# Performance work log

Hardware: AMD Instinct MI355X
Metric: run time of the kernel (lower is better)

The kernel has to match this reference:

```python
import jax, jax.numpy as jnp
import numpy as np
import math

D_MODEL = 1024
NUM_HEADS = 16
N_GROUP = 4
HEAD_DIM = D_MODEL // NUM_HEADS  # 64
KV_DIM = N_GROUP * HEAD_DIM      # 256
BS, SEQ = 2, 2048


def setup_inputs() -> dict:
    key = jax.random.key(0)
    ks = jax.random.split(key, 7)
    s = 0.02
    return {
        "h": jax.random.normal(ks[0], (BS, SEQ, D_MODEL), dtype=jnp.float32),
        "wq_w": jax.random.normal(ks[1], (D_MODEL, D_MODEL), dtype=jnp.float32) * s,
        "wq_b": jnp.zeros((D_MODEL,), dtype=jnp.float32),
        "wk_w": jax.random.normal(ks[2], (KV_DIM, D_MODEL), dtype=jnp.float32) * s,
        "wk_b": jnp.zeros((KV_DIM,), dtype=jnp.float32),
        "wv_w": jax.random.normal(ks[3], (KV_DIM, D_MODEL), dtype=jnp.float32) * s,
        "wv_b": jnp.zeros((KV_DIM,), dtype=jnp.float32),
    }


def reference(h, wq_w, wq_b, wk_w, wk_b, wv_w, wv_b):
    bs, seq, _ = h.shape
    rep = NUM_HEADS // N_GROUP  # heads per KV group

    # Linear projections (torch Linear: x @ W.T + b)
    q = h @ wq_w.T + wq_b                     # [bs, seq, d_model]
    k = h @ wk_w.T + wk_b                     # [bs, seq, kv_dim]
    v = h @ wv_w.T + wv_b                     # [bs, seq, kv_dim]

    q = q.reshape(bs, seq, NUM_HEADS, HEAD_DIM).transpose(0, 2, 1, 3)  # [b,H,s,d]
    k = k.reshape(bs, seq, N_GROUP, HEAD_DIM)                          # [b,s,G,d]
    v = v.reshape(bs, seq, N_GROUP, HEAD_DIM)
    # torch .repeat(1,1,1,rep).view(...,num_heads,head_dim) maps head h -> group h//rep,
    # identical to repeating each group `rep` times consecutively along the head axis.
    k = jnp.repeat(k, rep, axis=2).transpose(0, 2, 1, 3)               # [b,H,s,d]
    v = jnp.repeat(v, rep, axis=2).transpose(0, 2, 1, 3)               # [b,H,s,d]

    scores = jnp.einsum("bhqd,bhkd->bhqk", q, k) / math.sqrt(HEAD_DIM)
    attn = jax.nn.softmax(scores, axis=-1)
    out = jnp.einsum("bhqk,bhkd->bhqd", attn, v)                       # [b,H,s,d]
    out = out.transpose(0, 2, 1, 3).reshape(bs, seq, NUM_HEADS * HEAD_DIM)
    return out
```

## Files before the change

### kernel.cpp

```cpp
#include <hip/hip_runtime.h>

typedef _Float16 f16;
typedef _Float16 f16x8 __attribute__((ext_vector_type(8)));
typedef _Float16 f16x4 __attribute__((ext_vector_type(4)));
typedef float f32x4 __attribute__((ext_vector_type(4)));

#define MFMA16(a, b, c) __builtin_amdgcn_mfma_f32_16x16x32_f16((a), (b), (c), 0, 0, 0)

#define SEQ 2048
#define DMODEL 1024
#define NH 16
#define NG 4
#define PAD 76

__device__ __forceinline__ f16x8 cvt8(const float4 a, const float4 b) {
    f16x8 r;
    r[0] = (f16)a.x; r[1] = (f16)a.y; r[2] = (f16)a.z; r[3] = (f16)a.w;
    r[4] = (f16)b.x; r[5] = (f16)b.y; r[6] = (f16)b.z; r[7] = (f16)b.w;
    return r;
}

__device__ __forceinline__ void gl_lds16(f16* lds, const f16* g) {
    __builtin_amdgcn_global_load_lds(
        (const __attribute__((address_space(1))) void*)g,
        (__attribute__((address_space(3))) void*)lds, 16, 0, 0);
}

#define HN  (4096 * 1024)
#define WQN (1024 * 1024)
#define WKN (256 * 1024)
#define WVN (256 * 1024)
#define TOT8 ((HN + WQN + WKN + WVN) / 8)

__global__ __launch_bounds__(256) void cvt_kernel(const float* __restrict__ h,
                                                  const float* __restrict__ wq,
                                                  const float* __restrict__ wk,
                                                  const float* __restrict__ wv,
                                                  f16* __restrict__ h16,
                                                  f16* __restrict__ W16) {
    const int c = blockIdx.x * 256 + threadIdx.x;
    if (c >= TOT8) return;
    const size_t e = (size_t)c * 8;
    const float* src;
    f16* dst;
    if (e < HN) {
        src = h + e; dst = h16 + e;
    } else {
        const size_t e2 = e - HN;
        if (e2 < WQN)            src = wq + e2;
        else if (e2 < WQN + WKN) src = wk + (e2 - WQN);
        else                     src = wv + (e2 - WQN - WKN);
        dst = W16 + e2;
    }
    const float4 a = *(const float4*)src;
    const float4 b = *(const float4*)(src + 4);
    *(f16x8*)dst = cvt8(a, b);
}

__global__ __launch_bounds__(256, 3) void qkv_gemm16(const f16* __restrict__ A,
                                                     const f16* __restrict__ W,
                                                     const float* __restrict__ bq,
                                                     const float* __restrict__ bk,
                                                     const float* __restrict__ bv,
                                                     f16* __restrict__ Qb,
                                                     f16* __restrict__ Kb,
                                                     f16* __restrict__ Vtb,
                                                     float qscale) {
    __shared__ __align__(16) f16 As[2][64 * 32];
    __shared__ __align__(16) f16 Bs[2][128 * 32];

    const int tid  = threadIdx.x;
    const int lane = tid & 63;
    const int l15  = lane & 15;
    const int l4   = lane >> 4;
    const int wave = tid >> 6;
    const int wm   = (wave >> 1) * 32;
    const int wn   = (wave & 1) * 64;
    const int bx   = blockIdx.x;
    const int m0   = blockIdx.y * 64;
    const int n0g  = bx * 128;

    const f16* Ag = A + ((size_t)(m0 + (lane >> 2))) * 1024 + (lane & 3) * 8;
    const f16* Wg = W + ((size_t)(n0g + (lane >> 2))) * 1024 + (lane & 3) * 8;
    const size_t rstep = (size_t)16 * 1024;

    f32x4 acc[2][4];
#pragma unroll
    for (int i = 0; i < 2; i++)
#pragma unroll
        for (int j = 0; j < 4; j++) acc[i][j] = (f32x4)0.0f;

    gl_lds16(&As[0][wave * 512],        Ag + (size_t)wave * rstep);
    gl_lds16(&Bs[0][wave * 1024],       Wg + (size_t)(wave * 2) * rstep);
    gl_lds16(&Bs[0][wave * 1024 + 512], Wg + (size_t)(wave * 2 + 1) * rstep);

    int cur = 0;
    for (int k0 = 0; k0 < DMODEL; k0 += 32) {
        __syncthreads();
        if (k0 + 32 < DMODEL) {
            const int nxt = cur ^ 1;
            const int kn = k0 + 32;
            gl_lds16(&As[nxt][wave * 512],        Ag + (size_t)wave * rstep + kn);
            gl_lds16(&Bs[nxt][wave * 1024],       Wg + (size_t)(wave * 2) * rstep + kn);
            gl_lds16(&Bs[nxt][wave * 1024 + 512], Wg + (size_t)(wave * 2 + 1) * rstep + kn);
        }

        const f16* Ab = As[cur];
        const f16* Bb = Bs[cur];
        f16x8 af[2], bf[4];
#pragma unroll
        for (int i = 0; i < 2; i++)
            af[i] = *(const f16x8*)&Ab[(wm + i * 16 + l15) * 32 + l4 * 8];
#pragma unroll
        for (int j = 0; j < 4; j++)
            bf[j] = *(const f16x8*)&Bb[(wn + j * 16 + l15) * 32 + l4 * 8];
        __builtin_amdgcn_s_setprio(1);
#pragma unroll
        for (int i = 0; i < 2; i++)
#pragma unroll
            for (int j = 0; j < 4; j++)
                acc[i][j] = MFMA16(af[i], bf[j], acc[i][j]);
        __builtin_amdgcn_s_setprio(0);
        cur ^= 1;
    }

    const float* bias; f16* C; int N, n0; float osc; int vmode;
    if (bx < 8)       { bias = bq; C = Qb;  N = 1024; n0 = bx * 128;        osc = qscale; vmode = 0; }
    else if (bx < 10) { bias = bk; C = Kb;  N = 256;  n0 = (bx - 8) * 128;  osc = 1.0f;   vmode = 0; }
    else              { bias = bv; C = Vtb; N = 256;  n0 = (bx - 10) * 128; osc = 1.0f;   vmode = 1; }

#pragma unroll
    for (int i = 0; i < 2; i++) {
        const int mbase = m0 + wm + i * 16 + l4 * 4;
#pragma unroll
        for (int j = 0; j < 4; j++) {
            const int n  = n0 + wn + j * 16 + l15;
            const float bb = bias[n];
            if (vmode == 0) {
#pragma unroll
                for (int r = 0; r < 4; r++)
                    C[(size_t)(mbase + r) * N + n] = (f16)((acc[i][j][r] + bb) * osc);
            } else {
                f16x4 p;
#pragma unroll
                for (int r = 0; r < 4; r++)
                    p[r] = (f16)((acc[i][j][r] + bb) * osc);
                const int batch = mbase >> 11;
                const int s     = mbase & 2047;
                *(f16x4*)&C[((size_t)(batch * 256 + n)) * SEQ + s] = p;
            }
        }
    }
}

__global__ __launch_bounds__(256, 2) void attn_kernel(const f16* __restrict__ Q,
                                                      const f16* __restrict__ Kt,
                                                      const f16* __restrict__ Vt,
                                                      float* __restrict__ out) {
    __shared__ __align__(16) f16 Ks[64 * PAD];
    __shared__ __align__(16) f16 Vs[64 * PAD];
    __shared__ __align__(16) f16 Ps[128 * PAD];

    const int tid  = threadIdx.x;
    const int lane = tid & 63;
    const int l15  = lane & 15;
    const int l4   = lane >> 4;
    const int wave = tid >> 6;
    const int b    = blockIdx.z;
    const int hh   = blockIdx.y;
    const int g    = hh >> 2;
    const int q0   = blockIdx.x * 128;
    const int qw   = wave * 32;

    f16x8 qf[2][2];
#pragma unroll
    for (int rg = 0; rg < 2; rg++)
#pragma unroll
        for (int kt = 0; kt < 2; kt++)
            qf[rg][kt] = *(const f16x8*)&Q[((size_t)(b * SEQ + q0 + qw + rg * 16 + l15)) * DMODEL
                                           + hh * 64 + kt * 32 + l4 * 8];

    f32x4 oacc[2][4];
    float lsum[2] = {0.0f, 0.0f};
#pragma unroll
    for (int rg = 0; rg < 2; rg++)
#pragma unroll
        for (int dt = 0; dt < 4; dt++) oacc[rg][dt] = (f32x4)0.0f;

    const int srow = tid >> 2;
    const int sc8  = (tid & 3) * 8;
    const f16* Kg = Kt + (size_t)(b * SEQ + srow) * 256 + g * 64 + sc8;
    const f16* Vg = Vt + (size_t)(b * 256 + g * 64 + srow) * SEQ + sc8;

    for (int kb = 0; kb < SEQ; kb += 64) {
        *(f16x8*)&Ks[srow * PAD + sc8]      = *(const f16x8*)(Kg + (size_t)kb * 256);
        *(f16x8*)&Ks[srow * PAD + 32 + sc8] = *(const f16x8*)(Kg + (size_t)kb * 256 + 32);
        *(f16x8*)&Vs[srow * PAD + sc8]      = *(const f16x8*)(Vg + kb);
        *(f16x8*)&Vs[srow * PAD + 32 + sc8] = *(const f16x8*)(Vg + kb + 32);
        __syncthreads();

        f32x4 sacc[2][4];
#pragma unroll
        for (int rg = 0; rg < 2; rg++)
#pragma unroll
            for (int jt = 0; jt < 4; jt++) sacc[rg][jt] = (f32x4)0.0f;
#pragma unroll
        for (int jt = 0; jt < 4; jt++) {
            const f16x8 kf0 = *(const f16x8*)&Ks[(jt * 16 + l15) * PAD + l4 * 8];
            const f16x8 kf1 = *(const f16x8*)&Ks[(jt * 16 + l15) * PAD + 32 + l4 * 8];
#pragma unroll
            for (int rg = 0; rg < 2; rg++) {
                sacc[rg][jt] = MFMA16(kf0, qf[rg][0], sacc[rg][jt]);
                sacc[rg][jt] = MFMA16(kf1, qf[rg][1], sacc[rg][jt]);
            }
        }

#pragma unroll
        for (int rg = 0; rg < 2; rg++)
#pragma unroll
            for (int jt = 0; jt < 4; jt++) {
                f16x4 pp;
#pragma unroll
                for (int r = 0; r < 4; r++) {
                    const float p = exp2f(fminf(sacc[rg][jt][r], 14.0f));
                    lsum[rg] += p;
                    pp[r] = (f16)p;
                }
                *(f16x4*)&Ps[(qw + rg * 16 + l15) * PAD + jt * 16 + l4 * 4] = pp;
            }

#pragma unroll
        for (int kt = 0; kt < 2; kt++) {
            const f16x8 pf0 = *(const f16x8*)&Ps[(qw + l15) * PAD + kt * 32 + l4 * 8];
            const f16x8 pf1 = *(const f16x8*)&Ps[(qw + 16 + l15) * PAD + kt * 32 + l4 * 8];
#pragma unroll
            for (int dt = 0; dt < 4; dt++) {
                const f16x8 vf = *(const f16x8*)&Vs[(dt * 16 + l15) * PAD + kt * 32 + l4 * 8];
                oacc[0][dt] = MFMA16(pf0, vf, oacc[0][dt]);
                oacc[1][dt] = MFMA16(pf1, vf, oacc[1][dt]);
            }
        }
        __syncthreads();
    }

#pragma unroll
    for (int rg = 0; rg < 2; rg++) {
        lsum[rg] += __shfl_xor(lsum[rg], 16);
        lsum[rg] += __shfl_xor(lsum[rg], 32);
    }

#pragma unroll
    for (int rg = 0; rg < 2; rg++)
#pragma unroll
        for (int r = 0; r < 4; r++) {
            const float lv  = __shfl(lsum[rg], l4 * 4 + r);
            const float inv = 1.0f / lv;
            const int q = q0 + qw + rg * 16 + l4 * 4 + r;
            float* op = out + ((size_t)(b * SEQ + q)) * DMODEL + hh * 64;
#pragma unroll
            for (int dt = 0; dt < 4; dt++)
                op[dt * 16 + l15] = oacc[rg][dt][r] * inv;
        }
}

extern "C" void kernel_launch(void* const* d_in, const int* in_sizes, int n_in,
                              void* d_out, int out_size, void* d_ws, size_t ws_size,
                              hipStream_t stream) {
    const float* h    = (const float*)d_in[0];
    const float* wq_w = (const float*)d_in[1];
    const float* wq_b = (const float*)d_in[2];
    const float* wk_w = (const float*)d_in[3];
    const float* wk_b = (const float*)d_in[4];
    const float* wv_w = (const float*)d_in[5];
    const float* wv_b = (const float*)d_in[6];
    float* out = (float*)d_out;

    char* ws = (char*)d_ws;
    f16* Qb  = (f16*)(ws + 0);
    f16* Kb  = (f16*)(ws + 8388608);
    f16* Vtb = (f16*)(ws + 10485760);
    f16* h16 = (f16*)(ws + 12582912);
    f16* W16 = (f16*)(ws + 20971520);

    const float qscale = 0.125f * 1.4426950408889634f;

    cvt_kernel<<<dim3(TOT8 / 256), 256, 0, stream>>>(h, wq_w, wk_w, wv_w, h16, W16);
    qkv_gemm16<<<dim3(12, 64), 256, 0, stream>>>(h16, W16, wq_b, wk_b, wv_b,
                                                 Qb, Kb, Vtb, qscale);
    attn_kernel<<<dim3(16, 16, 2), 256, 0, stream>>>(Qb, Kb, Vtb, out);
}
```

Baseline: 182.0 us.

## Double-buffer K/V tiles in attention kernel with register prefetch

Splits the K and V shared-memory tiles into two buffers. The next tile is loaded from global memory into registers at the start of each iteration, while the current tile is used for the QK and PV MFMAs, and is written to the other buffer afterward. One __syncthreads per iteration is removed and load latency is meant to be hidden behind compute. The cost is more LDS (about 19KB extra per block) and 16 extra VGPRs, which could affect occupancy at 2 blocks per CU.

```diff
diff --git a/kernel.cpp b/kernel.cpp
--- a/kernel.cpp
+++ b/kernel.cpp
@@ -157,8 +157,8 @@
                                                       const f16* __restrict__ Kt,
                                                       const f16* __restrict__ Vt,
                                                       float* __restrict__ out) {
-    __shared__ __align__(16) f16 Ks[64 * PAD];
-    __shared__ __align__(16) f16 Vs[64 * PAD];
+    __shared__ __align__(16) f16 Ks[2][64 * PAD];
+    __shared__ __align__(16) f16 Vs[2][64 * PAD];
     __shared__ __align__(16) f16 Ps[128 * PAD];
 
     const int tid  = threadIdx.x;
@@ -192,12 +192,28 @@
     const f16* Kg = Kt + (size_t)(b * SEQ + srow) * 256 + g * 64 + sc8;
     const f16* Vg = Vt + (size_t)(b * 256 + g * 64 + srow) * SEQ + sc8;
 
+    {
+        const f16x8 k0 = *(const f16x8*)(Kg);
+        const f16x8 k1 = *(const f16x8*)(Kg + 32);
+        const f16x8 v0 = *(const f16x8*)(Vg);
+        const f16x8 v1 = *(const f16x8*)(Vg + 32);
+        *(f16x8*)&Ks[0][srow * PAD + sc8]      = k0;
+        *(f16x8*)&Ks[0][srow * PAD + 32 + sc8] = k1;
+        *(f16x8*)&Vs[0][srow * PAD + sc8]      = v0;
+        *(f16x8*)&Vs[0][srow * PAD + 32 + sc8] = v1;
+    }
+    __syncthreads();
+
+    int cur = 0;
     for (int kb = 0; kb < SEQ; kb += 64) {
-        *(f16x8*)&Ks[srow * PAD + sc8]      = *(const f16x8*)(Kg + (size_t)kb * 256);
-        *(f16x8*)&Ks[srow * PAD + 32 + sc8] = *(const f16x8*)(Kg + (size_t)kb * 256 + 32);
-        *(f16x8*)&Vs[srow * PAD + sc8]      = *(const f16x8*)(Vg + kb);
-        *(f16x8*)&Vs[srow * PAD + 32 + sc8] = *(const f16x8*)(Vg + kb + 32);
-        __syncthreads();
+        const bool more = (kb + 64) < SEQ;
+        f16x8 rk0, rk1, rv0, rv1;
+        if (more) {
+            rk0 = *(const f16x8*)(Kg + (size_t)(kb + 64) * 256);
+            rk1 = *(const f16x8*)(Kg + (size_t)(kb + 64) * 256 + 32);
+            rv0 = *(const f16x8*)(Vg + kb + 64);
+            rv1 = *(const f16x8*)(Vg + kb + 64 + 32);
+        }
 
         f32x4 sacc[2][4];
 #pragma unroll
@@ -206,8 +222,8 @@
             for (int jt = 0; jt < 4; jt++) sacc[rg][jt] = (f32x4)0.0f;
 #pragma unroll
         for (int jt = 0; jt < 4; jt++) {
-            const f16x8 kf0 = *(const f16x8*)&Ks[(jt * 16 + l15) * PAD + l4 * 8];
-            const f16x8 kf1 = *(const f16x8*)&Ks[(jt * 16 + l15) * PAD + 32 + l4 * 8];
+            const f16x8 kf0 = *(const f16x8*)&Ks[cur][(jt * 16 + l15) * PAD + l4 * 8];
+            const f16x8 kf1 = *(const f16x8*)&Ks[cur][(jt * 16 + l15) * PAD + 32 + l4 * 8];
 #pragma unroll
             for (int rg = 0; rg < 2; rg++) {
                 sacc[rg][jt] = MFMA16(kf0, qf[rg][0], sacc[rg][jt]);
@@ -235,12 +251,21 @@
             const f16x8 pf1 = *(const f16x8*)&Ps[(qw + 16 + l15) * PAD + kt * 32 + l4 * 8];
 #pragma unroll
             for (int dt = 0; dt < 4; dt++) {
-                const f16x8 vf = *(const f16x8*)&Vs[(dt * 16 + l15) * PAD + kt * 32 + l4 * 8];
+                const f16x8 vf = *(const f16x8*)&Vs[cur][(dt * 16 + l15) * PAD + kt * 32 + l4 * 8];
                 oacc[0][dt] = MFMA16(pf0, vf, oacc[0][dt]);
                 oacc[1][dt] = MFMA16(pf1, vf, oacc[1][dt]);
             }
         }
+
+        if (more) {
+            const int nxt = cur ^ 1;
+            *(f16x8*)&Ks[nxt][srow * PAD + sc8]      = rk0;
+            *(f16x8*)&Ks[nxt][srow * PAD + 32 + sc8] = rk1;
+            *(f16x8*)&Vs[nxt][srow * PAD + sc8]      = rv0;
+            *(f16x8*)&Vs[nxt][srow * PAD + 32 + sc8] = rv1;
+        }
         __syncthreads();
+        cur ^= 1;
     }
 
 #pragma unroll
```

Measured after the change: 175.2 us. 1.04x faster.

## Split KV range across waves, load K/V fragments directly to registers

Applied to the files above, without the earlier changes.

Each block now handles 64 queries; its four waves are split into two query halves and two KV halves (split-K), and partial outputs and row sums are merged through shared memory at the end. K and V tiles are no longer staged in LDS with per-iteration barriers. Each wave loads its MFMA fragments straight from global memory into registers, double-buffering K so the next tile's load overlaps the current compute. The grid doubles to 1024 blocks, which raises parallelism but reads K/V redundantly per wave from global/L2 and adds a reduction step.

```diff
diff --git a/kernel.cpp b/kernel.cpp
--- a/kernel.cpp
+++ b/kernel.cpp
@@ -153,24 +153,94 @@
     }
 }
 
+__device__ __forceinline__ void load_k(f16x8 (&dst)[2][4], const f16* __restrict__ Kg, int kb) {
+#pragma unroll
+    for (int jt = 0; jt < 4; jt++)
+#pragma unroll
+        for (int kt = 0; kt < 2; kt++)
+            dst[kt][jt] = *(const f16x8*)(Kg + (size_t)(kb + jt * 16) * 256 + kt * 32);
+}
+
+__device__ __forceinline__ void load_v(f16x8 (&dst)[2][4], const f16* __restrict__ Vg, int kb) {
+#pragma unroll
+    for (int dt = 0; dt < 4; dt++)
+#pragma unroll
+        for (int kt = 0; kt < 2; kt++)
+            dst[kt][dt] = *(const f16x8*)(Vg + (size_t)(dt * 16) * SEQ + kb + kt * 32);
+}
+
+__device__ __forceinline__ void attn_step(const f16x8 (&kc)[2][4], f16x8 (&kn)[2][4],
+                                          f16x8 (&vf)[2][4], const f16x8 (&qf)[2][2],
+                                          f32x4 (&oacc)[2][4], float (&lsum)[2],
+                                          f16* __restrict__ Ps,
+                                          const f16* __restrict__ Kg,
+                                          const f16* __restrict__ Vg,
+                                          int kb, int knext, int pw, int l15, int l4) {
+    load_v(vf, Vg, kb);
+
+    f32x4 sacc[2][4];
+#pragma unroll
+    for (int rg = 0; rg < 2; rg++)
+#pragma unroll
+        for (int jt = 0; jt < 4; jt++) sacc[rg][jt] = (f32x4)0.0f;
+#pragma unroll
+    for (int jt = 0; jt < 4; jt++)
+#pragma unroll
+        for (int rg = 0; rg < 2; rg++) {
+            sacc[rg][jt] = MFMA16(kc[0][jt], qf[rg][0], sacc[rg][jt]);
+            sacc[rg][jt] = MFMA16(kc[1][jt], qf[rg][1], sacc[rg][jt]);
+        }
+
+    load_k(kn, Kg, knext);
+
+#pragma unroll
+    for (int rg = 0; rg < 2; rg++)
+#pragma unroll
+        for (int jt = 0; jt < 4; jt++) {
+            f16x4 pp;
+#pragma unroll
+            for (int r = 0; r < 4; r++) {
+                const float p = exp2f(fminf(sacc[rg][jt][r], 14.0f));
+                lsum[rg] += p;
+                pp[r] = (f16)p;
+            }
+            *(f16x4*)&Ps[(pw + rg * 16 + l15) * PAD + jt * 16 + l4 * 4] = pp;
+        }
+
+#pragma unroll
+    for (int kt = 0; kt < 2; kt++) {
+        const f16x8 pf0 = *(const f16x8*)&Ps[(pw + l15) * PAD + kt * 32 + l4 * 8];
+        const f16x8 pf1 = *(const f16x8*)&Ps[(pw + 16 + l15) * PAD + kt * 32 + l4 * 8];
+#pragma unroll
+        for (int dt = 0; dt < 4; dt++) {
+            oacc[0][dt] = MFMA16(pf0, vf[kt][dt], oacc[0][dt]);
+            oacc[1][dt] = MFMA16(pf1, vf[kt][dt], oacc[1][dt]);
+        }
+    }
+}
+
 __global__ __launch_bounds__(256, 2) void attn_kernel(const f16* __restrict__ Q,
                                                       const f16* __restrict__ Kt,
                                                       const f16* __restrict__ Vt,
                                                       float* __restrict__ out) {
-    __shared__ __align__(16) f16 Ks[64 * PAD];
-    __shared__ __align__(16) f16 Vs[64 * PAD];
     __shared__ __align__(16) f16 Ps[128 * PAD];
+    __shared__ float Or[2][32][65];
+    __shared__ float Lr[2][32];
 
     const int tid  = threadIdx.x;
     const int lane = tid & 63;
     const int l15  = lane & 15;
     const int l4   = lane >> 4;
     const int wave = tid >> 6;
+    const int wq   = wave & 1;
+    const int wk   = wave >> 1;
     const int b    = blockIdx.z;
     const int hh   = blockIdx.y;
     const int g    = hh >> 2;
-    const int q0   = blockIdx.x * 128;
-    const int qw   = wave * 32;
+    const int q0   = blockIdx.x * 64;
+    const int qw   = wq * 32;
+    const int pw   = wave * 32;
+    const int kvbase = wk * 1024;
 
     f16x8 qf[2][2];
 #pragma unroll
@@ -187,60 +257,17 @@
 #pragma unroll
         for (int dt = 0; dt < 4; dt++) oacc[rg][dt] = (f32x4)0.0f;
 
-    const int srow = tid >> 2;
-    const int sc8  = (tid & 3) * 8;
-    const f16* Kg = Kt + (size_t)(b * SEQ + srow) * 256 + g * 64 + sc8;
-    const f16* Vg = Vt + (size_t)(b * 256 + g * 64 + srow) * SEQ + sc8;
-
-    for (int kb = 0; kb < SEQ; kb += 64) {
-        *(f16x8*)&Ks[srow * PAD + sc8]      = *(const f16x8*)(Kg + (size_t)kb * 256);
-        *(f16x8*)&Ks[srow * PAD + 32 + sc8] = *(const f16x8*)(Kg + (size_t)kb * 256 + 32);
-        *(f16x8*)&Vs[srow * PAD + sc8]      = *(const f16x8*)(Vg + kb);
-        *(f16x8*)&Vs[srow * PAD + 32 + sc8] = *(const f16x8*)(Vg + kb + 32);
-        __syncthreads();
-
-        f32x4 sacc[2][4];
-#pragma unroll
-        for (int rg = 0; rg < 2; rg++)
-#pragma unroll
-            for (int jt = 0; jt < 4; jt++) sacc[rg][jt] = (f32x4)0.0f;
-#pragma unroll
-        for (int jt = 0; jt < 4; jt++) {
-            const f16x8 kf0 = *(const f16x8*)&Ks[(jt * 16 + l15) * PAD + l4 * 8];
-            const f16x8 kf1 = *(const f16x8*)&Ks[(jt * 16 + l15) * PAD + 32 + l4 * 8];
-#pragma unroll
-            for (int rg = 0; rg < 2; rg++) {
-                sacc[rg][jt] = MFMA16(kf0, qf[rg][0], sacc[rg][jt]);
-                sacc[rg][jt] = MFMA16(kf1, qf[rg][1], sacc[rg][jt]);
-            }
-        }
-
-#pragma unroll
-        for (int rg = 0; rg < 2; rg++)
-#pragma unroll
-            for (int jt = 0; jt < 4; jt++) {
-                f16x4 pp;
-#pragma unroll
-                for (int r = 0; r < 4; r++) {
-                    const float p = exp2f(fminf(sacc[rg][jt][r], 14.0f));
-                    lsum[rg] += p;
-                    pp[r] = (f16)p;
-                }
-                *(f16x4*)&Ps[(qw + rg * 16 + l15) * PAD + jt * 16 + l4 * 4] = pp;
-            }
-
-#pragma unroll
-        for (int kt = 0; kt < 2; kt++) {
-            const f16x8 pf0 = *(const f16x8*)&Ps[(qw + l15) * PAD + kt * 32 + l4 * 8];
-            const f16x8 pf1 = *(const f16x8*)&Ps[(qw + 16 + l15) * PAD + kt * 32 + l4 * 8];
-#pragma unroll
-            for (int dt = 0; dt < 4; dt++) {
-                const f16x8 vf = *(const f16x8*)&Vs[(dt * 16 + l15) * PAD + kt * 32 + l4 * 8];
-                oacc[0][dt] = MFMA16(pf0, vf, oacc[0][dt]);
-                oacc[1][dt] = MFMA16(pf1, vf, oacc[1][dt]);
-            }
-        }
-        __syncthreads();
+    const f16* Kg = Kt + ((size_t)(b * SEQ) + l15) * 256 + g * 64 + l4 * 8;
+    const f16* Vg = Vt + ((size_t)(b * 256 + g * 64 + l15)) * SEQ + l4 * 8;
+
+    f16x8 kfA[2][4], kfB[2][4], vf[2][4];
+    load_k(kfA, Kg, kvbase);
+
+    for (int t2 = 0; t2 < 8; t2++) {
+        const int kb0 = kvbase + t2 * 128;
+        const int kn2 = (t2 == 7) ? kvbase : kb0 + 128;
+        attn_step(kfA, kfB, vf, qf, oacc, lsum, Ps, Kg, Vg, kb0,      kb0 + 64, pw, l15, l4);
+        attn_step(kfB, kfA, vf, qf, oacc, lsum, Ps, Kg, Vg, kb0 + 64, kn2,      pw, l15, l4);
     }
 
 #pragma unroll
@@ -249,18 +276,36 @@
         lsum[rg] += __shfl_xor(lsum[rg], 32);
     }
 
-#pragma unroll
-    for (int rg = 0; rg < 2; rg++)
-#pragma unroll
-        for (int r = 0; r < 4; r++) {
-            const float lv  = __shfl(lsum[rg], l4 * 4 + r);
-            const float inv = 1.0f / lv;
-            const int q = q0 + qw + rg * 16 + l4 * 4 + r;
-            float* op = out + ((size_t)(b * SEQ + q)) * DMODEL + hh * 64;
+    if (wk == 1) {
+#pragma unroll
+        for (int rg = 0; rg < 2; rg++)
 #pragma unroll
             for (int dt = 0; dt < 4; dt++)
-                op[dt * 16 + l15] = oacc[rg][dt][r] * inv;
-        }
+#pragma unroll
+                for (int r = 0; r < 4; r++)
+                    Or[wq][rg * 16 + l4 * 4 + r][dt * 16 + l15] = oacc[rg][dt][r];
+        if (l4 == 0) {
+#pragma unroll
+            for (int rg = 0; rg < 2; rg++)
+                Lr[wq][rg * 16 + l15] = lsum[rg];
+        }
+    }
+    __syncthreads();
+    if (wk == 0) {
+#pragma unroll
+        for (int rg = 0; rg < 2; rg++)
+#pragma unroll
+            for (int r = 0; r < 4; r++) {
+                const int qr = rg * 16 + l4 * 4 + r;
+                const float lv  = __shfl(lsum[rg], l4 * 4 + r) + Lr[wq][qr];
+                const float inv = 1.0f / lv;
+                const int q = q0 + qw + qr;
+                float* op = out + ((size_t)(b * SEQ + q)) * DMODEL + hh * 64;
+#pragma unroll
+                for (int dt = 0; dt < 4; dt++)
+                    op[dt * 16 + l15] = (oacc[rg][dt][r] + Or[wq][qr][dt * 16 + l15]) * inv;
+            }
+    }
 }
 
 extern "C" void kernel_launch(void* const* d_in, const int* in_sizes, int n_in,
@@ -287,5 +332,5 @@
     cvt_kernel<<<dim3(TOT8 / 256), 256, 0, stream>>>(h, wq_w, wk_w, wv_w, h16, W16);
     qkv_gemm16<<<dim3(12, 64), 256, 0, stream>>>(h16, W16, wq_b, wk_b, wv_b,
                                                  Qb, Kb, Vtb, qscale);
-    attn_kernel<<<dim3(16, 16, 2), 256, 0, stream>>>(Qb, Kb, Vtb, out);
-}
+    attn_kernel<<<dim3(32, 16, 2), 256, 0, stream>>>(Qb, Kb, Vtb, out);
+}
```

Measured after the change: 227.3 us. 24.9% more time.

## Split KV columns across waves in attention with async double-buffered LDS staging

Applied to the files above, without the earlier changes.

The attention kernel now gives each block 64 queries, and each of its four waves handles a different 16-key slice of every KV tile, rather than different query rows. The P matrix stays in registers and feeds a 16x16x16 MFMA directly, which removes the LDS round trip for P. K/V tiles are staged with global_load_lds into a double buffer so loads overlap compute, and the grid doubles. The cost is a cross-wave reduction of output accumulators and row sums through LDS scratch at the end, plus more accumulator registers per wave at a higher occupancy target.

```diff
diff --git a/kernel.cpp b/kernel.cpp
--- a/kernel.cpp
+++ b/kernel.cpp
@@ -5,7 +5,8 @@
 typedef _Float16 f16x4 __attribute__((ext_vector_type(4)));
 typedef float f32x4 __attribute__((ext_vector_type(4)));
 
-#define MFMA16(a, b, c) __builtin_amdgcn_mfma_f32_16x16x32_f16((a), (b), (c), 0, 0, 0)
+#define MFMA16(a, b, c)   __builtin_amdgcn_mfma_f32_16x16x32_f16((a), (b), (c), 0, 0, 0)
+#define MFMA16K(a, b, c)  __builtin_amdgcn_mfma_f32_16x16x16f16((a), (b), (c), 0, 0, 0)
 
 #define SEQ 2048
 #define DMODEL 1024
@@ -153,114 +154,149 @@
     }
 }
 
-__global__ __launch_bounds__(256, 2) void attn_kernel(const f16* __restrict__ Q,
+__global__ __launch_bounds__(256, 3) void attn_kernel(const f16* __restrict__ Q,
                                                       const f16* __restrict__ Kt,
                                                       const f16* __restrict__ Vt,
                                                       float* __restrict__ out) {
-    __shared__ __align__(16) f16 Ks[64 * PAD];
-    __shared__ __align__(16) f16 Vs[64 * PAD];
-    __shared__ __align__(16) f16 Ps[128 * PAD];
+    __shared__ __align__(16) f16 KV[2][2][2][64][32];
+    float* Scr = (float*)&KV[0][0][0][0][0];
+    float* Lr  = (float*)((char*)&KV[0][0][0][0][0] + 24576);
 
     const int tid  = threadIdx.x;
     const int lane = tid & 63;
     const int l15  = lane & 15;
     const int l4   = lane >> 4;
-    const int wave = tid >> 6;
+    const int w    = tid >> 6;
     const int b    = blockIdx.z;
     const int hh   = blockIdx.y;
     const int g    = hh >> 2;
-    const int q0   = blockIdx.x * 128;
-    const int qw   = wave * 32;
-
-    f16x8 qf[2][2];
-#pragma unroll
-    for (int rg = 0; rg < 2; rg++)
+    const int q0   = blockIdx.x * 64;
+
+    f16x8 qf[4][2];
+#pragma unroll
+    for (int rg = 0; rg < 4; rg++)
 #pragma unroll
         for (int kt = 0; kt < 2; kt++)
-            qf[rg][kt] = *(const f16x8*)&Q[((size_t)(b * SEQ + q0 + qw + rg * 16 + l15)) * DMODEL
+            qf[rg][kt] = *(const f16x8*)&Q[((size_t)(b * SEQ + q0 + rg * 16 + l15)) * DMODEL
                                            + hh * 64 + kt * 32 + l4 * 8];
 
-    f32x4 oacc[2][4];
-    float lsum[2] = {0.0f, 0.0f};
-#pragma unroll
-    for (int rg = 0; rg < 2; rg++)
+    f32x4 oacc[4][4];
+    float lsum[4] = {0.0f, 0.0f, 0.0f, 0.0f};
+#pragma unroll
+    for (int rg = 0; rg < 4; rg++)
 #pragma unroll
         for (int dt = 0; dt < 4; dt++) oacc[rg][dt] = (f32x4)0.0f;
 
-    const int srow = tid >> 2;
-    const int sc8  = (tid & 3) * 8;
-    const f16* Kg = Kt + (size_t)(b * SEQ + srow) * 256 + g * 64 + sc8;
-    const f16* Vg = Vt + (size_t)(b * 256 + g * 64 + srow) * SEQ + sc8;
-
-    for (int kb = 0; kb < SEQ; kb += 64) {
-        *(f16x8*)&Ks[srow * PAD + sc8]      = *(const f16x8*)(Kg + (size_t)kb * 256);
-        *(f16x8*)&Ks[srow * PAD + 32 + sc8] = *(const f16x8*)(Kg + (size_t)kb * 256 + 32);
-        *(f16x8*)&Vs[srow * PAD + sc8]      = *(const f16x8*)(Vg + kb);
-        *(f16x8*)&Vs[srow * PAD + 32 + sc8] = *(const f16x8*)(Vg + kb + 32);
+    const int gr = lane >> 2;
+    const int gc = (lane & 3) * 8;
+    const f16* Kg = Kt + ((size_t)(b * SEQ + w * 16 + gr)) * 256 + g * 64 + gc;
+    const f16* Vg = Vt + ((size_t)(b * 256 + g * 64 + w * 16 + gr)) * SEQ + gc;
+
+#define STAGE(buf, kb)                                                          \
+    do {                                                                        \
+        gl_lds16(&KV[buf][0][0][w * 16][0], Kg + (size_t)(kb) * 256);           \
+        gl_lds16(&KV[buf][0][1][w * 16][0], Kg + (size_t)(kb) * 256 + 32);      \
+        gl_lds16(&KV[buf][1][0][w * 16][0], Vg + (kb));                         \
+        gl_lds16(&KV[buf][1][1][w * 16][0], Vg + (kb) + 32);                    \
+    } while (0)
+
+    STAGE(0, 0);
+    __syncthreads();
+
+    int cur = 0;
+    for (int t = 0; t < 32; t++) {
+        if (t < 31) STAGE(cur ^ 1, (t + 1) * 64);
+
+        const f16x8 kf0 = *(const f16x8*)&KV[cur][0][0][w * 16 + l15][l4 * 8];
+        const f16x8 kf1 = *(const f16x8*)&KV[cur][0][1][w * 16 + l15][l4 * 8];
+
+        f32x4 sacc[4];
+#pragma unroll
+        for (int rg = 0; rg < 4; rg++) sacc[rg] = (f32x4)0.0f;
+#pragma unroll
+        for (int rg = 0; rg < 4; rg++) {
+            sacc[rg] = MFMA16(kf0, qf[rg][0], sacc[rg]);
+            sacc[rg] = MFMA16(kf1, qf[rg][1], sacc[rg]);
+        }
+
+        f16x4 pa[4];
+#pragma unroll
+        for (int rg = 0; rg < 4; rg++)
+#pragma unroll
+            for (int r = 0; r < 4; r++) {
+                const float p = exp2f(fminf(sacc[rg][r], 14.0f));
+                lsum[rg] += p;
+                pa[rg][r] = (f16)p;
+            }
+
+#pragma unroll
+        for (int dt = 0; dt < 4; dt++) {
+            const f16x4 vf = *(const f16x4*)&KV[cur][1][w >> 1][dt * 16 + l15][(w & 1) * 16 + l4 * 4];
+#pragma unroll
+            for (int rg = 0; rg < 4; rg++)
+                oacc[rg][dt] = MFMA16K(pa[rg], vf, oacc[rg][dt]);
+        }
+
         __syncthreads();
-
-        f32x4 sacc[2][4];
-#pragma unroll
-        for (int rg = 0; rg < 2; rg++)
-#pragma unroll
-            for (int jt = 0; jt < 4; jt++) sacc[rg][jt] = (f32x4)0.0f;
-#pragma unroll
-        for (int jt = 0; jt < 4; jt++) {
-            const f16x8 kf0 = *(const f16x8*)&Ks[(jt * 16 + l15) * PAD + l4 * 8];
-            const f16x8 kf1 = *(const f16x8*)&Ks[(jt * 16 + l15) * PAD + 32 + l4 * 8];
-#pragma unroll
-            for (int rg = 0; rg < 2; rg++) {
-                sacc[rg][jt] = MFMA16(kf0, qf[rg][0], sacc[rg][jt]);
-                sacc[rg][jt] = MFMA16(kf1, qf[rg][1], sacc[rg][jt]);
-            }
-        }
-
-#pragma unroll
-        for (int rg = 0; rg < 2; rg++)
-#pragma unroll
-            for (int jt = 0; jt < 4; jt++) {
-                f16x4 pp;
-#pragma unroll
-                for (int r = 0; r < 4; r++) {
-                    const float p = exp2f(fminf(sacc[rg][jt][r], 14.0f));
-                    lsum[rg] += p;
-                    pp[r] = (f16)p;
-                }
-                *(f16x4*)&Ps[(qw + rg * 16 + l15) * PAD + jt * 16 + l4 * 4] = pp;
-            }
-
-#pragma unroll
-        for (int kt = 0; kt < 2; kt++) {
-            const f16x8 pf0 = *(const f16x8*)&Ps[(qw + l15) * PAD + kt * 32 + l4 * 8];
-            const f16x8 pf1 = *(const f16x8*)&Ps[(qw + 16 + l15) * PAD + kt * 32 + l4 * 8];
-#pragma unroll
-            for (int dt = 0; dt < 4; dt++) {
-                const f16x8 vf = *(const f16x8*)&Vs[(dt * 16 + l15) * PAD + kt * 32 + l4 * 8];
-                oacc[0][dt] = MFMA16(pf0, vf, oacc[0][dt]);
-                oacc[1][dt] = MFMA16(pf1, vf, oacc[1][dt]);
-            }
-        }
-        __syncthreads();
-    }
-
-#pragma unroll
-    for (int rg = 0; rg < 2; rg++) {
+        cur ^= 1;
+    }
+
+#pragma unroll
+    for (int rg = 0; rg < 4; rg++) {
         lsum[rg] += __shfl_xor(lsum[rg], 16);
         lsum[rg] += __shfl_xor(lsum[rg], 32);
     }
-
-#pragma unroll
-    for (int rg = 0; rg < 2; rg++)
-#pragma unroll
-        for (int r = 0; r < 4; r++) {
-            const float lv  = __shfl(lsum[rg], l4 * 4 + r);
-            const float inv = 1.0f / lv;
-            const int q = q0 + qw + rg * 16 + l4 * 4 + r;
-            float* op = out + ((size_t)(b * SEQ + q)) * DMODEL + hh * 64;
-#pragma unroll
-            for (int dt = 0; dt < 4; dt++)
-                op[dt * 16 + l15] = oacc[rg][dt][r] * inv;
-        }
+    if (l4 == 0) {
+#pragma unroll
+        for (int rg = 0; rg < 4; rg++)
+            Lr[w * 64 + rg * 16 + l15] = lsum[rg];
+    }
+    __syncthreads();
+    float ltot[4];
+#pragma unroll
+    for (int rg = 0; rg < 4; rg++)
+        ltot[rg] = Lr[0 * 64 + rg * 16 + l15] + Lr[1 * 64 + rg * 16 + l15]
+                 + Lr[2 * 64 + rg * 16 + l15] + Lr[3 * 64 + rg * 16 + l15];
+
+    for (int h = 0; h < 2; h++) {
+        __syncthreads();
+        if (w > 0) {
+#pragma unroll
+            for (int rgl = 0; rgl < 2; rgl++) {
+                const int rg = h * 2 + rgl;
+#pragma unroll
+                for (int dt = 0; dt < 4; dt++)
+#pragma unroll
+                    for (int r = 0; r < 4; r++)
+                        Scr[((size_t)(w - 1) * 32 + rgl * 16 + l4 * 4 + r) * 64 + dt * 16 + l15]
+                            = oacc[rg][dt][r];
+            }
+        }
+        __syncthreads();
+        if (w == 0) {
+#pragma unroll
+            for (int rgl = 0; rgl < 2; rgl++) {
+                const int rg = h * 2 + rgl;
+#pragma unroll
+                for (int r = 0; r < 4; r++) {
+                    const float lv  = __shfl(ltot[rg], l4 * 4 + r);
+                    const float inv = 1.0f / lv;
+                    const int q = q0 + rg * 16 + l4 * 4 + r;
+                    float* op = out + ((size_t)(b * SEQ + q)) * DMODEL + hh * 64;
+#pragma unroll
+                    for (int dt = 0; dt < 4; dt++) {
+                        const size_t si = ((size_t)0 * 32 + rgl * 16 + l4 * 4 + r) * 64 + dt * 16 + l15;
+                        const float v = oacc[rg][dt][r]
+                                      + Scr[si]
+                                      + Scr[si + (size_t)32 * 64]
+                                      + Scr[si + (size_t)64 * 64];
+                        op[dt * 16 + l15] = v * inv;
+                    }
+                }
+            }
+        }
+    }
+#undef STAGE
 }
 
 extern "C" void kernel_launch(void* const* d_in, const int* in_sizes, int n_in,
@@ -287,5 +323,5 @@
     cvt_kernel<<<dim3(TOT8 / 256), 256, 0, stream>>>(h, wq_w, wk_w, wv_w, h16, W16);
     qkv_gemm16<<<dim3(12, 64), 256, 0, stream>>>(h16, W16, wq_b, wk_b, wv_b,
                                                  Qb, Kb, Vtb, qscale);
-    attn_kernel<<<dim3(16, 16, 2), 256, 0, stream>>>(Qb, Kb, Vtb, out);
-}
+    attn_kernel<<<dim3(32, 16, 2), 256, 0, stream>>>(Qb, Kb, Vtb, out);
+}
```

Result: no change. 183.9 us (+1.0%).
